# Optimization experiments

Hardware: AMD Instinct MI355X
Metric: run time of the kernel (lower is better)

## Reference

```python
import jax, jax.numpy as jnp
import numpy as np

B, LI, LT = 1, 2048, 256
HID, HEADS, HD = 3072, 24, 128
MLP = 4 * HID  # 12288
EPS = 1e-6


def setup_inputs() -> dict:
    key = jax.random.key(0)
    ks = jax.random.split(key, 12)
    n = lambda k, s, sc=1.0: jax.random.normal(k, s, dtype=jnp.float32) * sc
    # RoPE tables, interleaved-pair layout over head_dim
    theta = 10000.0 ** (-jnp.arange(0, HD, 2, dtype=jnp.float32) / HD)  # [HD/2]
    ang = jnp.arange(LI, dtype=jnp.float32)[:, None] * theta[None, :]   # [LI, HD/2]
    freqs_cos = jnp.repeat(jnp.cos(ang), 2, axis=-1)  # [LI, HD]
    freqs_sin = jnp.repeat(jnp.sin(ang), 2, axis=-1)
    return {
        "img": n(ks[0], (B, LI, HID)),
        "txt": n(ks[1], (B, LT, HID)),
        "vec": n(ks[2], (B, HID)),
        "freqs_cos": freqs_cos,
        "freqs_sin": freqs_sin,
        "w1": n(ks[3], (3 * HID + MLP, HID), 0.02),
        "b1": jnp.zeros((3 * HID + MLP,), jnp.float32),
        "w2": n(ks[4], (HID, HID + MLP), 0.02),
        "b2": jnp.zeros((HID,), jnp.float32),
        "q_norm_w": jnp.ones((HD,), jnp.float32),
        "k_norm_w": jnp.ones((HD,), jnp.float32),
        "mod_w": n(ks[5], (3 * HID, HID), 0.02),
        "mod_b": jnp.zeros((3 * HID,), jnp.float32),
        "txt_len": LT,
    }


def _layernorm(x):  # no affine, eps=1e-6
    mu = x.mean(-1, keepdims=True)
    var = ((x - mu) ** 2).mean(-1, keepdims=True)
    return (x - mu) * jax.lax.rsqrt(var + EPS)


def _rmsnorm(x, w):  # per-head-dim RMSNorm with affine weight
    ms = (x * x).mean(-1, keepdims=True)
    return x * jax.lax.rsqrt(ms + EPS) * w


def _rope(x, cos, sin):  # x: [B,L,H,D]; interleaved complex rotation
    xr = x.reshape(*x.shape[:-1], HD // 2, 2)
    rot = jnp.stack([-xr[..., 1], xr[..., 0]], axis=-1).reshape(x.shape)
    return x * cos[None, :, None, :] + rot * sin[None, :, None, :]


def reference(img, txt, vec, freqs_cos, freqs_sin, w1, b1, w2, b2,
              q_norm_w, k_norm_w, mod_w, mod_b, txt_len):
    H = img.shape[-1]
    Li = img.shape[1]
    # modulation: SiLU(vec) @ W -> shift, scale, gate
    mod = jax.nn.silu(vec) @ mod_w.T + mod_b           # [B, 3H]
    shift, scale, gate = jnp.split(mod, 3, axis=-1)
    modulate = lambda x: x * (1.0 + scale[:, None, :]) + shift[:, None, :]
    img_mod = modulate(_layernorm(img))
    txt_mod = modulate(_layernorm(txt))
    x_mod = jnp.concatenate([img_mod, txt_mod], axis=1)  # [B,S,H]
    Bb, S = x_mod.shape[0], x_mod.shape[1]
    # fused QKV projection (slices of linear1)
    qkv = x_mod @ w1[: 3 * H].T + b1[: 3 * H]
    q, k, v = [t.reshape(Bb, S, HEADS, HD) for t in jnp.split(qkv, 3, axis=-1)]
    q = _rmsnorm(q, q_norm_w)
    k = _rmsnorm(k, k_norm_w)
    # RoPE only on the img portion of the sequence
    q = jnp.concatenate([_rope(q[:, :Li], freqs_cos, freqs_sin), q[:, Li:]], axis=1)
    k = jnp.concatenate([_rope(k[:, :Li], freqs_cos, freqs_sin), k[:, Li:]], axis=1)
    # full (non-causal) attention over img+txt tokens
    logits = jnp.einsum('bqhd,bkhd->bhqk', q, k) * (HD ** -0.5)
    probs = jax.nn.softmax(logits, axis=-1)
    attn = jnp.einsum('bhqk,bkhd->bqhd', probs, v).reshape(Bb, S, H)
    # MLP branch (linear1 mlp slice) with gelu-tanh, then fused linear2
    mlp = jax.nn.gelu(x_mod @ w1[3 * H:].T + b1[3 * H:], approximate=True)
    out = jnp.concatenate([attn, mlp], axis=-1) @ w2.T + b2  # [B,S,H]
    img_out = img + gate[:, None, :] * out[:, :-txt_len]
    txt_out = txt + gate[:, None, :] * out[:, -txt_len:]
    return img_out, txt_out
```

## Files before the change

kernel.cpp:

```cpp
#include <hip/hip_runtime.h>
#include <hip/hip_bf16.h>

#define DI __device__ __forceinline__

typedef __attribute__((ext_vector_type(8))) short bf8;
typedef __attribute__((ext_vector_type(4))) float f4;
typedef __attribute__((ext_vector_type(8))) unsigned short us8;

#define LI    2048
#define LT    256
#define SEQ   2304
#define HID   3072
#define NHEAD 24
#define HD    128
#define N1    21504
#define QKVW  9216
#define N2CAT 15360

DI unsigned short f2bf(float f) {
  union { float f; unsigned u; } v; v.f = f;
  unsigned r = v.u + 0x7FFFu + ((v.u >> 16) & 1u);
  return (unsigned short)(r >> 16);
}
DI float bf2f(unsigned short h) {
  union { unsigned u; float f; } v; v.u = ((unsigned)h) << 16;
  return v.f;
}

DI void gload16(const void* g, void* l) {
  __builtin_amdgcn_global_load_lds(
      (const __attribute__((address_space(1))) void*)g,
      (__attribute__((address_space(3))) void*)l, 16, 0, 0);
}

DI f4 mfma16(bf8 a, bf8 b, f4 c) {
  return __builtin_amdgcn_mfma_f32_16x16x32_bf16(a, b, c, 0, 0, 0);
}

__global__ void k_mod(const float* __restrict__ vec, const float* __restrict__ mw,
                      const float* __restrict__ mb, float* __restrict__ mod) {
  int row = blockIdx.x * 4 + (threadIdx.x >> 6);
  int lane = threadIdx.x & 63;
  const float4* wr = (const float4*)(mw + (size_t)row * HID);
  const float4* vv = (const float4*)vec;
  float s = 0.f;
  for (int i = lane; i < HID / 4; i += 64) {
    float4 w4 = wr[i], x4 = vv[i];
    s += (x4.x / (1.f + __expf(-x4.x))) * w4.x;
    s += (x4.y / (1.f + __expf(-x4.y))) * w4.y;
    s += (x4.z / (1.f + __expf(-x4.z))) * w4.z;
    s += (x4.w / (1.f + __expf(-x4.w))) * w4.w;
  }
#pragma unroll
  for (int m = 32; m; m >>= 1) s += __shfl_xor(s, m);
  if (lane == 0) mod[row] = s + mb[row];
}

__global__ void k_lnmod(const float* __restrict__ img, const float* __restrict__ txt,
                        const float* __restrict__ mod, unsigned short* __restrict__ xmod) {
  int t = blockIdx.x;
  const float* x = (t < LI) ? (img + (size_t)t * HID) : (txt + (size_t)(t - LI) * HID);
  const float4* x4 = (const float4*)x;
  float4 v[3];
  float s = 0.f, ss = 0.f;
#pragma unroll
  for (int j = 0; j < 3; ++j) {
    v[j] = x4[threadIdx.x + j * 256];
    s  += v[j].x + v[j].y + v[j].z + v[j].w;
    ss += v[j].x * v[j].x + v[j].y * v[j].y + v[j].z * v[j].z + v[j].w * v[j].w;
  }
#pragma unroll
  for (int m = 32; m; m >>= 1) { s += __shfl_xor(s, m); ss += __shfl_xor(ss, m); }
  __shared__ float red[8];
  int wv = threadIdx.x >> 6;
  if ((threadIdx.x & 63) == 0) { red[wv] = s; red[4 + wv] = ss; }
  __syncthreads();
  s = red[0] + red[1] + red[2] + red[3];
  ss = red[4] + red[5] + red[6] + red[7];
  float mu = s * (1.f / HID);
  float var = ss * (1.f / HID) - mu * mu;
  float inv = rsqrtf(var + 1e-6f);
  const float* shift = mod;
  const float* scale = mod + HID;
#pragma unroll
  for (int j = 0; j < 3; ++j) {
    int i = threadIdx.x + j * 256;
    int c = i * 4;
    ushort4 o;
    o.x = f2bf((v[j].x - mu) * inv * (1.f + scale[c + 0]) + shift[c + 0]);
    o.y = f2bf((v[j].y - mu) * inv * (1.f + scale[c + 1]) + shift[c + 1]);
    o.z = f2bf((v[j].z - mu) * inv * (1.f + scale[c + 2]) + shift[c + 2]);
    o.w = f2bf((v[j].w - mu) * inv * (1.f + scale[c + 3]) + shift[c + 3]);
    ((ushort4*)xmod)[(size_t)t * (HID / 4) + i] = o;
  }
}

__global__ void k_f2bf(const float* __restrict__ in, unsigned short* __restrict__ out, int n4) {
  int stride = gridDim.x * blockDim.x;
  for (int i = blockIdx.x * blockDim.x + threadIdx.x; i < n4; i += stride) {
    float4 f = ((const float4*)in)[i];
    ushort4 o;
    o.x = f2bf(f.x); o.y = f2bf(f.y); o.z = f2bf(f.z); o.w = f2bf(f.w);
    ((ushort4*)out)[i] = o;
  }
}

#define BAR()    asm volatile("s_barrier" ::: "memory")
#define VMCNT2() asm volatile("s_waitcnt vmcnt(2)" ::: "memory")
#define VMCNT0() asm volatile("s_waitcnt vmcnt(0)" ::: "memory")
#define LGKM0()  do { asm volatile("s_waitcnt lgkmcnt(0)" ::: "memory"); \
                      __builtin_amdgcn_sched_barrier(0); } while (0)

__global__ __launch_bounds__(512, 2) void k_gemm1(const unsigned short* __restrict__ xmod,
    const unsigned short* __restrict__ w1b, const float* __restrict__ b1,
    unsigned short* __restrict__ qkv, unsigned short* __restrict__ amlp) {
  __shared__ unsigned short As[2][256 * 64];
  __shared__ unsigned short Bs[2][256 * 64];
  const int K = HID;
  const int NT = K / 64;
  int tid = threadIdx.x, lane = tid & 63, wid = tid >> 6;
  int wr = wid >> 2, wc = wid & 3;

  int b = blockIdx.x;
  const int Q = 756 / 8, R = 756 % 8;
  int xcd = b & 7, idx = b >> 3;
  int wg = (xcd < R ? xcd * (Q + 1) : R * (Q + 1) + (xcd - R) * Q) + idx;
  int bm = wg % 9, bn = wg / 9;

  const unsigned short* Ag = xmod + (size_t)bm * 256 * K;
  const unsigned short* Bg = w1b + (size_t)bn * 256 * K;

  int sgran = (lane & 7) ^ ((lane >> 3) & 7);
  int srow = wid * 16 + (lane >> 3);

#define STAGE_A(bufi, t, hh) do { \
    gload16(Ag + (size_t)((hh)*128 + srow) * K + (t)*64 + sgran*8, \
            &As[bufi][((hh)*128 + wid*16) * 64]); \
    gload16(Ag + (size_t)((hh)*128 + 8 + srow) * K + (t)*64 + sgran*8, \
            &As[bufi][((hh)*128 + wid*16 + 8) * 64]); \
  } while (0)
#define STAGE_B(bufi, t, hh) do { \
    gload16(Bg + (size_t)((hh)*128 + srow) * K + (t)*64 + sgran*8, \
            &Bs[bufi][((hh)*128 + wid*16) * 64]); \
    gload16(Bg + (size_t)((hh)*128 + 8 + srow) * K + (t)*64 + sgran*8, \
            &Bs[bufi][((hh)*128 + wid*16 + 8) * 64]); \
  } while (0)

  int rA = wr * 128 + (lane & 15);
  int rB = wc * 64 + (lane & 15);
  int qq = lane >> 4, l7 = lane & 7;

  f4 acc[8][4];
#pragma unroll
  for (int m = 0; m < 8; ++m)
#pragma unroll
    for (int n = 0; n < 4; ++n) acc[m][n] = (f4){0.f, 0.f, 0.f, 0.f};
  bf8 aL[4][2], aH[4][2], bL[2][2], bH[2][2];

#define RD(buf, r, s) (*(const bf8*)&buf[(r) * 64 + ((((s)*4 + qq) ^ l7) << 3)])

#define GROUP(C, tt, tn, tn2) do { \
     \
    _Pragma("unroll") for (int m = 0; m < 4; ++m) \
      _Pragma("unroll") for (int s = 0; s < 2; ++s) aL[m][s] = RD(As[C], rA + m*16, s); \
    _Pragma("unroll") for (int n = 0; n < 2; ++n) \
      _Pragma("unroll") for (int s = 0; s < 2; ++s) bL[n][s] = RD(Bs[C], rB + n*16, s); \
    STAGE_A(1-(C), tn, 1); \
    LGKM0(); \
    __builtin_amdgcn_s_setprio(1); \
    _Pragma("unroll") for (int m = 0; m < 4; ++m) \
      _Pragma("unroll") for (int n = 0; n < 2; ++n) \
        _Pragma("unroll") for (int s = 0; s < 2; ++s) \
          acc[m][n] = mfma16(aL[m][s], bL[n][s], acc[m][n]); \
    __builtin_amdgcn_s_setprio(0); \
    BAR(); \
     \
    _Pragma("unroll") for (int n = 0; n < 2; ++n) \
      _Pragma("unroll") for (int s = 0; s < 2; ++s) bH[n][s] = RD(Bs[C], rB + (n+2)*16, s); \
    STAGE_B(1-(C), tn, 0); \
    LGKM0(); \
    __builtin_amdgcn_s_setprio(1); \
    _Pragma("unroll") for (int m = 0; m < 4; ++m) \
      _Pragma("unroll") for (int n = 0; n < 2; ++n) \
        _Pragma("unroll") for (int s = 0; s < 2; ++s) \
          acc[m][n+2] = mfma16(aL[m][s], bH[n][s], acc[m][n+2]); \
    __builtin_amdgcn_s_setprio(0); \
    BAR(); \
     \
    _Pragma("unroll") for (int m = 0; m < 4; ++m) \
      _Pragma("unroll") for (int s = 0; s < 2; ++s) aH[m][s] = RD(As[C], rA + (m+4)*16, s); \
    STAGE_B(1-(C), tn, 1); \
    LGKM0(); \
    __builtin_amdgcn_s_setprio(1); \
    _Pragma("unroll") for (int m = 0; m < 4; ++m) \
      _Pragma("unroll") for (int n = 0; n < 2; ++n) \
        _Pragma("unroll") for (int s = 0; s < 2; ++s) \
          acc[m+4][n+2] = mfma16(aH[m][s], bH[n][s], acc[m+4][n+2]); \
    __builtin_amdgcn_s_setprio(0); \
    BAR(); \
     \
    STAGE_A(C, tn2, 0); \
    __builtin_amdgcn_s_setprio(1); \
    _Pragma("unroll") for (int m = 0; m < 4; ++m) \
      _Pragma("unroll") for (int n = 0; n < 2; ++n) \
        _Pragma("unroll") for (int s = 0; s < 2; ++s) \
          acc[m+4][n] = mfma16(aH[m][s], bL[n][s], acc[m+4][n]); \
    __builtin_amdgcn_s_setprio(0); \
    VMCNT2();    \
    BAR(); \
  } while (0)

  STAGE_A(0, 0, 0); STAGE_A(0, 0, 1); STAGE_B(0, 0, 0); STAGE_B(0, 0, 1);
  STAGE_A(1, 1, 0);
  VMCNT2();
  BAR();

  for (int i = 0; i < NT / 2; ++i) {
    int t0 = 2 * i, t1 = 2 * i + 1;
    int n1 = t0 + 2; if (n1 > NT - 1) n1 = NT - 1;
    int n2 = t0 + 3; if (n2 > NT - 1) n2 = NT - 1;
    GROUP(0, t0, t0 + 1, n1);
    GROUP(1, t1, n1, n2);
  }
  VMCNT0();

  int r0 = bm * 256 + wr * 128 + ((lane >> 4) << 2);
  int c0 = bn * 256 + wc * 64 + (lane & 15);
  bool isqkv = (bn * 256) < QKVW;
#pragma unroll
  for (int m = 0; m < 8; ++m) {
#pragma unroll
    for (int n = 0; n < 4; ++n) {
      int col = c0 + n * 16;
      float bias = b1[col];
#pragma unroll
      for (int j = 0; j < 4; ++j) {
        int row = r0 + m * 16 + j;
        float v = acc[m][n][j] + bias;
        if (isqkv) {
          qkv[(size_t)row * QKVW + col] = f2bf(v);
        } else {
          float u = 0.7978845608f * (v + 0.044715f * v * v * v);
          float g = v / (1.f + __expf(-2.f * u));
          amlp[(size_t)row * N2CAT + (col - 6144)] = f2bf(g);
        }
      }
    }
  }
#undef STAGE_A
#undef STAGE_B
#undef RD
#undef GROUP
}

DI void gemm_core(const unsigned short* __restrict__ A, const unsigned short* __restrict__ Bw,
                  int K, int bm, int bn, unsigned short* As, unsigned short* Bs, f4 acc[4][4]) {
  int tid = threadIdx.x;
  int lane = tid & 63;
  int wr = (tid >> 7) & 1;
  int wc = (tid >> 6) & 1;
#pragma unroll
  for (int m = 0; m < 4; ++m)
#pragma unroll
    for (int n = 0; n < 4; ++n) acc[m][n] = (f4){0.f, 0.f, 0.f, 0.f};

  int rbase = tid >> 3;
  int slg = (tid & 7) ^ (rbase & 7);
  const unsigned short* Ag = A + (size_t)(bm * 128 + rbase) * K + slg * 8;
  const unsigned short* Bg = Bw + (size_t)(bn * 128 + rbase) * K + slg * 8;
  unsigned short* Asd = As + tid * 8;
  unsigned short* Bsd = Bs + tid * 8;

  int rA = wr * 64 + (lane & 15);
  int rB = wc * 64 + (lane & 15);
  int cb = (lane >> 4) * 8;
  int cx = (lane & 7) << 3;

  for (int k0 = 0; k0 < K; k0 += 64) {
    __syncthreads();
#pragma unroll
    for (int j = 0; j < 4; ++j) {
      gload16(Ag + (size_t)(j * 32) * K + k0, Asd + j * 2048);
      gload16(Bg + (size_t)(j * 32) * K + k0, Bsd + j * 2048);
    }
    __syncthreads();
#pragma unroll
    for (int kk = 0; kk < 2; ++kk) {
      bf8 av[4], bv[4];
#pragma unroll
      for (int m = 0; m < 4; ++m)
        av[m] = *(const bf8*)&As[(rA + m * 16) * 64 + ((kk * 32 + cb) ^ cx)];
#pragma unroll
      for (int n = 0; n < 4; ++n)
        bv[n] = *(const bf8*)&Bs[(rB + n * 16) * 64 + ((kk * 32 + cb) ^ cx)];
#pragma unroll
      for (int m = 0; m < 4; ++m)
#pragma unroll
        for (int n = 0; n < 4; ++n)
          acc[m][n] = mfma16(av[m], bv[n], acc[m][n]);
    }
  }
}

__global__ __launch_bounds__(256) void k_gemm2(const unsigned short* __restrict__ amlp,
    const unsigned short* __restrict__ w2b, const float* __restrict__ b2,
    const float* __restrict__ img, const float* __restrict__ txt,
    const float* __restrict__ gate, float* __restrict__ out) {
  __shared__ unsigned short As[128 * 64], Bs[128 * 64];
  int nb = gridDim.x;
  int b = blockIdx.x;
  int bsw = (b & 7) * (nb >> 3) + (b >> 3);
  int bm = bsw % 18, bn = bsw / 18;
  f4 acc[4][4];
  gemm_core(amlp, w2b, N2CAT, bm, bn, As, Bs, acc);
  int lane = threadIdx.x & 63;
  int wr = (threadIdx.x >> 7) & 1, wc = (threadIdx.x >> 6) & 1;
  int r0 = bm * 128 + wr * 64 + ((lane >> 4) << 2);
  int c0 = bn * 128 + wc * 64 + (lane & 15);
#pragma unroll
  for (int m = 0; m < 4; ++m) {
#pragma unroll
    for (int n = 0; n < 4; ++n) {
      int col = c0 + n * 16;
      float bias = b2[col];
      float gt = gate[col];
#pragma unroll
      for (int j = 0; j < 4; ++j) {
        int row = r0 + m * 16 + j;
        float v = acc[m][n][j] + bias;
        float res = (row < LI) ? img[(size_t)row * HID + col]
                               : txt[(size_t)(row - LI) * HID + col];
        out[(size_t)row * HID + col] = res + gt * v;
      }
    }
  }
}

__global__ void k_qknorm(unsigned short* __restrict__ qkv, const float* __restrict__ qw,
                         const float* __restrict__ kw, const float* __restrict__ fcos,
                         const float* __restrict__ fsin) {
  int gw = (blockIdx.x * 256 + threadIdx.x) >> 6;
  int lane = threadIdx.x & 63;
  int token = gw / NHEAD, head = gw - token * NHEAD;
  bool dorope = token < LI;
  float c = 1.f, sn = 0.f;
  if (dorope) { c = fcos[token * HD + 2 * lane]; sn = fsin[token * HD + 2 * lane]; }
#pragma unroll
  for (int qk = 0; qk < 2; ++qk) {
    unsigned short* p = qkv + (size_t)token * QKVW + qk * HID + head * HD;
    unsigned u = ((const unsigned*)p)[lane];
    float x0 = bf2f((unsigned short)(u & 0xffff));
    float x1 = bf2f((unsigned short)(u >> 16));
    float ss = x0 * x0 + x1 * x1;
#pragma unroll
    for (int m2 = 32; m2; m2 >>= 1) ss += __shfl_xor(ss, m2);
    float inv = rsqrtf(ss * (1.f / HD) + 1e-6f);
    const float* w = qk ? kw : qw;
    float y0 = x0 * inv * w[2 * lane];
    float y1 = x1 * inv * w[2 * lane + 1];
    if (dorope) { float r0 = y0 * c - y1 * sn; float r1 = y1 * c + y0 * sn; y0 = r0; y1 = r1; }
    ((unsigned*)p)[lane] = ((unsigned)f2bf(y0)) | (((unsigned)f2bf(y1)) << 16);
  }
}

__global__ void k_vt(const unsigned short* __restrict__ qkv, unsigned short* __restrict__ vt) {
  int b = blockIdx.x;
  int h = b / 72; int rem = b - h * 72; int tt = rem >> 1; int dd = rem & 1;
  int t0 = tt * 64, d0 = dd * 64;
  __shared__ unsigned short tile[64 * 65];
  int tid = threadIdx.x;
#pragma unroll
  for (int j = 0; j < 2; ++j) {
    int idx = j * 256 + tid;
    int row = idx >> 3, s = idx & 7;
    us8 vv = *(const us8*)(qkv + (size_t)(t0 + row) * QKVW + 2 * HID + h * HD + d0 + s * 8);
#pragma unroll
    for (int i = 0; i < 8; ++i) tile[row * 65 + s * 8 + i] = vv[i];
  }
  __syncthreads();
#pragma unroll
  for (int j = 0; j < 2; ++j) {
    int idx = j * 256 + tid;
    int dr = idx >> 3, sl = idx & 7;
    us8 o;
#pragma unroll
    for (int i = 0; i < 8; ++i) o[i] = tile[(sl * 8 + i) * 65 + dr];
    *(us8*)(vt + (size_t)(h * HD + d0 + dr) * SEQ + t0 + sl * 8) = o;
  }
}

__global__ __launch_bounds__(256) void k_attn(const unsigned short* __restrict__ qkv,
                                              const unsigned short* __restrict__ vt,
                                              unsigned short* __restrict__ amlp) {
  int b = blockIdx.x;
  int bsw = (b & 7) * 108 + (b >> 3);
  int head = bsw / 36, qt = bsw - head * 36;
  int tid = threadIdx.x, lane = tid & 63, wv = tid >> 6;
  __shared__ unsigned short Qs[64 * 128], Ks[64 * 128], Vs[128 * 64], Ps[64 * 64];
  int qbase = qt * 64;

  {
    int row = tid >> 4, sl = tid & 15;
    int slg = sl ^ (row & 7);
    const unsigned short* qg = qkv + (size_t)(qbase + row) * QKVW + head * HD + slg * 8;
#pragma unroll
    for (int j = 0; j < 4; ++j)
      gload16(qg + (size_t)(j * 16) * QKVW, &Qs[(j * 256 + tid) * 8]);
  }

  float mrun[4], lrun[4];
  f4 oacc[8];
#pragma unroll
  for (int j = 0; j < 4; ++j) { mrun[j] = -1e30f; lrun[j] = 0.f; }
#pragma unroll
  for (int n = 0; n < 8; ++n) oacc[n] = (f4){0.f, 0.f, 0.f, 0.f};
  bf8 qf[4];

  for (int kt = 0; kt < SEQ / 64; ++kt) {
    __syncthreads();
    {
      int rloc = tid >> 4, sl = tid & 15, slg = sl ^ (rloc & 7);
      const unsigned short* kg =
          qkv + HID + (size_t)(kt * 64 + rloc) * QKVW + head * HD + slg * 8;
#pragma unroll
      for (int j = 0; j < 4; ++j) gload16(kg + (size_t)(j * 16) * QKVW, &Ks[(j * 256 + tid) * 8]);
    }
    {
      int rloc = tid >> 3, sl = tid & 7, slg = sl ^ (rloc & 7);
      const unsigned short* vg = vt + (size_t)(head * HD + rloc) * SEQ + kt * 64 + slg * 8;
#pragma unroll
      for (int j = 0; j < 4; ++j) gload16(vg + (size_t)(j * 32) * SEQ, &Vs[(j * 256 + tid) * 8]);
    }
    __syncthreads();
    if (kt == 0) {
#pragma unroll
      for (int kk = 0; kk < 4; ++kk) {
        int row = wv * 16 + (lane & 15);
        int col = (kk * 32 + ((lane >> 4) * 8)) ^ ((lane & 7) << 3);
        qf[kk] = *(const bf8*)&Qs[row * 128 + col];
      }
    }
    f4 sacc[4];
#pragma unroll
    for (int n = 0; n < 4; ++n) sacc[n] = (f4){0.f, 0.f, 0.f, 0.f};
#pragma unroll
    for (int kk = 0; kk < 4; ++kk) {
#pragma unroll
      for (int n = 0; n < 4; ++n) {
        int row = n * 16 + (lane & 15);
        int col = (kk * 32 + ((lane >> 4) * 8)) ^ ((lane & 7) << 3);
        bf8 kf = *(const bf8*)&Ks[row * 128 + col];
        sacc[n] = mfma16(qf[kk], kf, sacc[n]);
      }
    }
    const float SC = 0.08838834764831845f;
    float mj[4];
#pragma unroll
    for (int j = 0; j < 4; ++j)
      mj[j] = fmaxf(fmaxf(sacc[0][j], sacc[1][j]), fmaxf(sacc[2][j], sacc[3][j]));
#pragma unroll
    for (int j = 0; j < 4; ++j) {
#pragma unroll
      for (int mk = 8; mk; mk >>= 1) mj[j] = fmaxf(mj[j], __shfl_xor(mj[j], mk));
    }
    float resc[4], psum[4];
#pragma unroll
    for (int j = 0; j < 4; ++j) {
      float nm = fmaxf(mrun[j], mj[j] * SC);
      resc[j] = __expf(mrun[j] - nm);
      mrun[j] = nm;
      psum[j] = 0.f;
    }
#pragma unroll
    for (int n = 0; n < 4; ++n) {
#pragma unroll
      for (int j = 0; j < 4; ++j) {
        float p = __expf(sacc[n][j] * SC - mrun[j]);
        psum[j] += p;
        int row = wv * 16 + ((lane >> 4) << 2) + j;
        int col = (n * 16 + (lane & 15)) ^ ((row & 7) << 3);
        Ps[row * 64 + col] = f2bf(p);
      }
    }
#pragma unroll
    for (int j = 0; j < 4; ++j) {
#pragma unroll
      for (int mk = 8; mk; mk >>= 1) psum[j] += __shfl_xor(psum[j], mk);
      lrun[j] = lrun[j] * resc[j] + psum[j];
    }
#pragma unroll
    for (int n = 0; n < 8; ++n) {
#pragma unroll
      for (int j = 0; j < 4; ++j) oacc[n][j] *= resc[j];
    }
#pragma unroll
    for (int kk = 0; kk < 2; ++kk) {
      int prow = wv * 16 + (lane & 15);
      int pcol = (kk * 32 + ((lane >> 4) * 8)) ^ ((lane & 7) << 3);
      bf8 pa = *(const bf8*)&Ps[prow * 64 + pcol];
#pragma unroll
      for (int n = 0; n < 8; ++n) {
        int vrow = n * 16 + (lane & 15);
        int vcol = (kk * 32 + ((lane >> 4) * 8)) ^ ((vrow & 7) << 3);
        bf8 vf = *(const bf8*)&Vs[vrow * 64 + vcol];
        oacc[n] = mfma16(pa, vf, oacc[n]);
      }
    }
  }
#pragma unroll
  for (int j = 0; j < 4; ++j) {
    float invl = 1.f / lrun[j];
    int row = qbase + wv * 16 + ((lane >> 4) << 2) + j;
#pragma unroll
    for (int n = 0; n < 8; ++n) {
      int col = head * HD + n * 16 + (lane & 15);
      amlp[(size_t)row * N2CAT + col] = f2bf(oacc[n][j] * invl);
    }
  }
}

extern "C" void kernel_launch(void* const* d_in, const int* in_sizes, int n_in,
                              void* d_out, int out_size, void* d_ws, size_t ws_size,
                              hipStream_t stream) {
  (void)in_sizes; (void)n_in; (void)out_size; (void)ws_size;
  const float* img  = (const float*)d_in[0];
  const float* txt  = (const float*)d_in[1];
  const float* vec  = (const float*)d_in[2];
  const float* fcos = (const float*)d_in[3];
  const float* fsin = (const float*)d_in[4];
  const float* w1   = (const float*)d_in[5];
  const float* b1   = (const float*)d_in[6];
  const float* w2   = (const float*)d_in[7];
  const float* b2   = (const float*)d_in[8];
  const float* qnw  = (const float*)d_in[9];
  const float* knw  = (const float*)d_in[10];
  const float* mw   = (const float*)d_in[11];
  const float* mb   = (const float*)d_in[12];
  float* out = (float*)d_out;

  char* ws = (char*)d_ws;
  float*          mod  = (float*)(ws);
  unsigned short* xmod = (unsigned short*)(ws + 40960);
  unsigned short* w1b  = (unsigned short*)(ws + 14196736);
  unsigned short* qkv  = (unsigned short*)(ws + 146317312);
  unsigned short* amlp = (unsigned short*)(ws + 188784640);
  unsigned short* vtb  = xmod;
  unsigned short* w2b  = w1b;

  k_mod<<<QKVW / 4, 256, 0, stream>>>(vec, mw, mb, mod);
  k_lnmod<<<SEQ, 256, 0, stream>>>(img, txt, mod, xmod);
  k_f2bf<<<2048, 256, 0, stream>>>(w1, w1b, N1 * HID / 4);
  k_gemm1<<<756, 512, 0, stream>>>(xmod, w1b, b1, qkv, amlp);
  k_qknorm<<<SEQ * NHEAD / 4, 256, 0, stream>>>(qkv, qnw, knw, fcos, fsin);
  k_vt<<<NHEAD * 36 * 2, 256, 0, stream>>>(qkv, vtb);
  k_f2bf<<<2048, 256, 0, stream>>>(w2, w2b, HID * N2CAT / 4);
  k_attn<<<864, 256, 0, stream>>>(qkv, vtb, amlp);
  k_gemm2<<<18 * 24, 256, 0, stream>>>(amlp, w2b, b2, img, txt, mod + 2 * HID, out);
}
```

Baseline: 983.8 us.

## Rewrite gemm2 as triple-buffered 256x128 tile pipeline with interleaved async loads

The second GEMM (attn+mlp concat times w2) moves from a simple 128x128 single-buffer loop with two syncthreads per k-step to a 512-thread, 256x128 tile kernel. It uses a three-stage LDS ring, and loads for tile t+2 are issued between MFMA groups under vmcnt waits, so global memory latency overlaps compute. The grid becomes 216 blocks with an XCD-aware swizzle. gemm1 also has one B staging load moved earlier in its group. The larger tile and deeper buffering raise LDS use per block, and 216 blocks may not fill every CU evenly.

```diff
diff --git a/kernel.cpp b/kernel.cpp
--- a/kernel.cpp
+++ b/kernel.cpp
@@ -106,6 +106,7 @@
 }
 
 #define BAR()    asm volatile("s_barrier" ::: "memory")
+#define VMCNT6() asm volatile("s_waitcnt vmcnt(6)" ::: "memory")
 #define VMCNT2() asm volatile("s_waitcnt vmcnt(2)" ::: "memory")
 #define VMCNT0() asm volatile("s_waitcnt vmcnt(0)" ::: "memory")
 #define LGKM0()  do { asm volatile("s_waitcnt lgkmcnt(0)" ::: "memory"); \
@@ -160,7 +161,6 @@
 #define RD(buf, r, s) (*(const bf8*)&buf[(r) * 64 + ((((s)*4 + qq) ^ l7) << 3)])
 
 #define GROUP(C, tt, tn, tn2) do { \
-     \
     _Pragma("unroll") for (int m = 0; m < 4; ++m) \
       _Pragma("unroll") for (int s = 0; s < 2; ++s) aL[m][s] = RD(As[C], rA + m*16, s); \
     _Pragma("unroll") for (int n = 0; n < 2; ++n) \
@@ -174,10 +174,10 @@
           acc[m][n] = mfma16(aL[m][s], bL[n][s], acc[m][n]); \
     __builtin_amdgcn_s_setprio(0); \
     BAR(); \
-     \
     _Pragma("unroll") for (int n = 0; n < 2; ++n) \
       _Pragma("unroll") for (int s = 0; s < 2; ++s) bH[n][s] = RD(Bs[C], rB + (n+2)*16, s); \
     STAGE_B(1-(C), tn, 0); \
+    STAGE_B(1-(C), tn, 1); \
     LGKM0(); \
     __builtin_amdgcn_s_setprio(1); \
     _Pragma("unroll") for (int m = 0; m < 4; ++m) \
@@ -186,10 +186,8 @@
           acc[m][n+2] = mfma16(aL[m][s], bH[n][s], acc[m][n+2]); \
     __builtin_amdgcn_s_setprio(0); \
     BAR(); \
-     \
     _Pragma("unroll") for (int m = 0; m < 4; ++m) \
       _Pragma("unroll") for (int s = 0; s < 2; ++s) aH[m][s] = RD(As[C], rA + (m+4)*16, s); \
-    STAGE_B(1-(C), tn, 1); \
     LGKM0(); \
     __builtin_amdgcn_s_setprio(1); \
     _Pragma("unroll") for (int m = 0; m < 4; ++m) \
@@ -198,7 +196,6 @@
           acc[m+4][n+2] = mfma16(aH[m][s], bH[n][s], acc[m+4][n+2]); \
     __builtin_amdgcn_s_setprio(0); \
     BAR(); \
-     \
     STAGE_A(C, tn2, 0); \
     __builtin_amdgcn_s_setprio(1); \
     _Pragma("unroll") for (int m = 0; m < 4; ++m) \
@@ -206,7 +203,7 @@
         _Pragma("unroll") for (int s = 0; s < 2; ++s) \
           acc[m+4][n] = mfma16(aH[m][s], bL[n][s], acc[m+4][n]); \
     __builtin_amdgcn_s_setprio(0); \
-    VMCNT2();    \
+    VMCNT2(); \
     BAR(); \
   } while (0)
 
@@ -253,69 +250,117 @@
 #undef GROUP
 }
 
-DI void gemm_core(const unsigned short* __restrict__ A, const unsigned short* __restrict__ Bw,
-                  int K, int bm, int bn, unsigned short* As, unsigned short* Bs, f4 acc[4][4]) {
-  int tid = threadIdx.x;
-  int lane = tid & 63;
-  int wr = (tid >> 7) & 1;
-  int wc = (tid >> 6) & 1;
-#pragma unroll
-  for (int m = 0; m < 4; ++m)
-#pragma unroll
-    for (int n = 0; n < 4; ++n) acc[m][n] = (f4){0.f, 0.f, 0.f, 0.f};
-
-  int rbase = tid >> 3;
-  int slg = (tid & 7) ^ (rbase & 7);
-  const unsigned short* Ag = A + (size_t)(bm * 128 + rbase) * K + slg * 8;
-  const unsigned short* Bg = Bw + (size_t)(bn * 128 + rbase) * K + slg * 8;
-  unsigned short* Asd = As + tid * 8;
-  unsigned short* Bsd = Bs + tid * 8;
-
-  int rA = wr * 64 + (lane & 15);
-  int rB = wc * 64 + (lane & 15);
-  int cb = (lane >> 4) * 8;
-  int cx = (lane & 7) << 3;
-
-  for (int k0 = 0; k0 < K; k0 += 64) {
-    __syncthreads();
-#pragma unroll
-    for (int j = 0; j < 4; ++j) {
-      gload16(Ag + (size_t)(j * 32) * K + k0, Asd + j * 2048);
-      gload16(Bg + (size_t)(j * 32) * K + k0, Bsd + j * 2048);
-    }
-    __syncthreads();
-#pragma unroll
-    for (int kk = 0; kk < 2; ++kk) {
-      bf8 av[4], bv[4];
-#pragma unroll
-      for (int m = 0; m < 4; ++m)
-        av[m] = *(const bf8*)&As[(rA + m * 16) * 64 + ((kk * 32 + cb) ^ cx)];
-#pragma unroll
-      for (int n = 0; n < 4; ++n)
-        bv[n] = *(const bf8*)&Bs[(rB + n * 16) * 64 + ((kk * 32 + cb) ^ cx)];
-#pragma unroll
-      for (int m = 0; m < 4; ++m)
-#pragma unroll
-        for (int n = 0; n < 4; ++n)
-          acc[m][n] = mfma16(av[m], bv[n], acc[m][n]);
-    }
-  }
-}
-
-__global__ __launch_bounds__(256) void k_gemm2(const unsigned short* __restrict__ amlp,
+__global__ __launch_bounds__(512, 2) void k_gemm2(const unsigned short* __restrict__ amlp,
     const unsigned short* __restrict__ w2b, const float* __restrict__ b2,
     const float* __restrict__ img, const float* __restrict__ txt,
     const float* __restrict__ gate, float* __restrict__ out) {
-  __shared__ unsigned short As[128 * 64], Bs[128 * 64];
-  int nb = gridDim.x;
+  __shared__ unsigned short As[3][256 * 64];
+  __shared__ unsigned short Bs[3][128 * 64];
+  const int K = N2CAT;
+  const int NT = K / 64;
+  int tid = threadIdx.x, lane = tid & 63, wid = tid >> 6;
+  int wr = wid >> 1, wc = wid & 1;
+
   int b = blockIdx.x;
-  int bsw = (b & 7) * (nb >> 3) + (b >> 3);
-  int bm = bsw % 18, bn = bsw / 18;
+  int bsw = (b & 7) * 27 + (b >> 3);
+  int bm = bsw % 9, bn = bsw / 9;
+
+  const unsigned short* Ag = amlp + (size_t)bm * 256 * K;
+  const unsigned short* Bg = w2b + (size_t)bn * 128 * K;
+
+  int sgran = (lane & 7) ^ ((lane >> 3) & 7);
+  int srow = wid * 16 + (lane >> 3);
+
+#define STAGE2_A(bufi, t, hh) do { \
+    gload16(Ag + (size_t)((hh)*128 + srow) * K + (t)*64 + sgran*8, \
+            &As[bufi][((hh)*128 + wid*16) * 64]); \
+    gload16(Ag + (size_t)((hh)*128 + 8 + srow) * K + (t)*64 + sgran*8, \
+            &As[bufi][((hh)*128 + wid*16 + 8) * 64]); \
+  } while (0)
+#define STAGE2_B(bufi, t) do { \
+    gload16(Bg + (size_t)(srow) * K + (t)*64 + sgran*8, \
+            &Bs[bufi][(wid*16) * 64]); \
+    gload16(Bg + (size_t)(8 + srow) * K + (t)*64 + sgran*8, \
+            &Bs[bufi][(wid*16 + 8) * 64]); \
+  } while (0)
+
+  int rA = wr * 64 + (lane & 15);
+  int rB = wc * 64 + (lane & 15);
+  int qq = lane >> 4, l7 = lane & 7;
+
   f4 acc[4][4];
-  gemm_core(amlp, w2b, N2CAT, bm, bn, As, Bs, acc);
-  int lane = threadIdx.x & 63;
-  int wr = (threadIdx.x >> 7) & 1, wc = (threadIdx.x >> 6) & 1;
-  int r0 = bm * 128 + wr * 64 + ((lane >> 4) << 2);
+#pragma unroll
+  for (int m = 0; m < 4; ++m)
+#pragma unroll
+    for (int n = 0; n < 4; ++n) acc[m][n] = (f4){0.f, 0.f, 0.f, 0.f};
+  bf8 aL[2][2], aH[2][2], bL[2][2], bH[2][2];
+
+#define RD2(buf, r, s) (*(const bf8*)&buf[(r) * 64 + ((((s)*4 + qq) ^ l7) << 3)])
+
+#define GROUP2(C, SB, t, full) do { \
+     \
+    _Pragma("unroll") for (int m = 0; m < 2; ++m) \
+      _Pragma("unroll") for (int s = 0; s < 2; ++s) aL[m][s] = RD2(As[C], rA + m*16, s); \
+    _Pragma("unroll") for (int n = 0; n < 2; ++n) \
+      _Pragma("unroll") for (int s = 0; s < 2; ++s) bL[n][s] = RD2(Bs[C], rB + n*16, s); \
+    if (full) STAGE2_A(SB, (t) + 2, 0); \
+    LGKM0(); \
+    __builtin_amdgcn_s_setprio(1); \
+    _Pragma("unroll") for (int m = 0; m < 2; ++m) \
+      _Pragma("unroll") for (int n = 0; n < 2; ++n) \
+        _Pragma("unroll") for (int s = 0; s < 2; ++s) \
+          acc[m][n] = mfma16(aL[m][s], bL[n][s], acc[m][n]); \
+    __builtin_amdgcn_s_setprio(0); \
+    BAR(); \
+     \
+    _Pragma("unroll") for (int n = 0; n < 2; ++n) \
+      _Pragma("unroll") for (int s = 0; s < 2; ++s) bH[n][s] = RD2(Bs[C], rB + (n+2)*16, s); \
+    if (full) STAGE2_A(SB, (t) + 2, 1); \
+    LGKM0(); \
+    __builtin_amdgcn_s_setprio(1); \
+    _Pragma("unroll") for (int m = 0; m < 2; ++m) \
+      _Pragma("unroll") for (int n = 0; n < 2; ++n) \
+        _Pragma("unroll") for (int s = 0; s < 2; ++s) \
+          acc[m][n+2] = mfma16(aL[m][s], bH[n][s], acc[m][n+2]); \
+    __builtin_amdgcn_s_setprio(0); \
+    BAR(); \
+     \
+    _Pragma("unroll") for (int m = 0; m < 2; ++m) \
+      _Pragma("unroll") for (int s = 0; s < 2; ++s) aH[m][s] = RD2(As[C], rA + (m+2)*16, s); \
+    if (full) STAGE2_B(SB, (t) + 2); \
+    LGKM0(); \
+    __builtin_amdgcn_s_setprio(1); \
+    _Pragma("unroll") for (int m = 0; m < 2; ++m) \
+      _Pragma("unroll") for (int n = 0; n < 2; ++n) \
+        _Pragma("unroll") for (int s = 0; s < 2; ++s) \
+          acc[m+2][n+2] = mfma16(aH[m][s], bH[n][s], acc[m+2][n+2]); \
+    __builtin_amdgcn_s_setprio(0); \
+    BAR(); \
+     \
+    __builtin_amdgcn_s_setprio(1); \
+    _Pragma("unroll") for (int m = 0; m < 2; ++m) \
+      _Pragma("unroll") for (int n = 0; n < 2; ++n) \
+        _Pragma("unroll") for (int s = 0; s < 2; ++s) \
+          acc[m+2][n] = mfma16(aH[m][s], bL[n][s], acc[m+2][n]); \
+    __builtin_amdgcn_s_setprio(0); \
+    if (full) { VMCNT6(); } else { VMCNT0(); } \
+    BAR(); \
+  } while (0)
+
+  STAGE2_A(0, 0, 0); STAGE2_A(0, 0, 1); STAGE2_B(0, 0);
+  STAGE2_A(1, 1, 0); STAGE2_A(1, 1, 1); STAGE2_B(1, 1);
+  VMCNT6();
+  BAR();
+
+  for (int i = 0; i < NT / 3; ++i) {
+    int t = 3 * i;
+    GROUP2(0, 2, t,     (t + 2) < NT);
+    GROUP2(1, 0, t + 1, (t + 3) < NT);
+    GROUP2(2, 1, t + 2, (t + 4) < NT);
+  }
+  VMCNT0();
+
+  int r0 = bm * 256 + wr * 64 + ((lane >> 4) << 2);
   int c0 = bn * 128 + wc * 64 + (lane & 15);
 #pragma unroll
   for (int m = 0; m < 4; ++m) {
@@ -334,6 +379,10 @@
       }
     }
   }
+#undef STAGE2_A
+#undef STAGE2_B
+#undef RD2
+#undef GROUP2
 }
 
 __global__ void k_qknorm(unsigned short* __restrict__ qkv, const float* __restrict__ qw,
@@ -555,5 +604,5 @@
   k_vt<<<NHEAD * 36 * 2, 256, 0, stream>>>(qkv, vtb);
   k_f2bf<<<2048, 256, 0, stream>>>(w2, w2b, HID * N2CAT / 4);
   k_attn<<<864, 256, 0, stream>>>(qkv, vtb, amlp);
-  k_gemm2<<<18 * 24, 256, 0, stream>>>(amlp, w2b, b2, img, txt, mod + 2 * HID, out);
-}
+  k_gemm2<<<216, 512, 0, stream>>>(amlp, w2b, b2, img, txt, mod + 2 * HID, out);
+}
```

After: 965.7 us. No clear change (-1.8%).
